# Kernel optimization log

Hardware: AMD Instinct MI355X
Metric: run time of the kernel (lower is better)

The kernel has to match this reference:

```python
import jax, jax.numpy as jnp
import numpy as np

GRID = 32
NUM_VOXELS = GRID ** 3


def setup_inputs() -> dict:
    key = jax.random.key(0)
    k1, k2 = jax.random.split(key)
    B, D, N = 4, 128, 100000
    features = jax.random.normal(k1, (B, D, N), dtype=jnp.float32)
    xyz = jax.random.uniform(k2, (B, N, 3), dtype=jnp.float32)
    return {"features": features, "xyz": xyz}


def reference(features, xyz):
    # features: [B, D, N], xyz: [B, N, 3]
    B, D, N = features.shape
    G, V = GRID, NUM_VOXELS
    xyz_min = jnp.min(xyz, axis=1, keepdims=True)          # [B, 1, 3]
    xyz_max = jnp.max(xyz, axis=1, keepdims=True)          # [B, 1, 3]
    xyz_range = xyz_max - xyz_min + 1e-8
    norm = jnp.clip((xyz - xyz_min) / xyz_range, 0.0, 1.0 - 1e-6)
    vi = jnp.clip(jnp.floor(norm * G).astype(jnp.int32), 0, G - 1)  # [B, N, 3]
    idx = vi[..., 0] * (G * G) + vi[..., 1] * G + vi[..., 2]        # [B, N]

    def per_batch(feat, ix):
        # feat: [D, N], ix: [N]
        counts = jnp.zeros((V,), jnp.int32).at[ix].add(1)
        # scatter-max, include_self=False semantics: init -inf, then
        # empty voxels fall back to 0 (torch leaves initial zeros untouched)
        fmax = jnp.full((V, feat.shape[0]), -jnp.inf, feat.dtype).at[ix].max(feat.T)
        fmax = jnp.where(counts[:, None] == 0, jnp.zeros((), feat.dtype), fmax)
        return counts, fmax.T  # [V], [D, V]

    counts, voxel_features = jax.vmap(per_batch)(features, idx)
    voxel_features_3d = voxel_features.reshape(B, D, G, G, G)
    point_counts = counts[:, None, :].astype(jnp.int64)     # [B, 1, V]
    xyz_min_out = jnp.swapaxes(xyz_min, 1, 2)               # [B, 3, 1]
    xyz_max_out = jnp.swapaxes(xyz_max, 1, 2)
    return (voxel_features_3d, idx, point_counts, xyz_min_out, xyz_max_out)
```

## Files before the change

### kernel.cpp

```cpp
#include <hip/hip_runtime.h>
#include <math.h>

#define GG 32
#define NV (GG * GG * GG)
#define BB 4
#define DD 128

__device__ __forceinline__ unsigned int enc_f(float f) {
    unsigned int u = __float_as_uint(f);
    return (u & 0x80000000u) ? ~u : (u | 0x80000000u);
}
__device__ __forceinline__ float dec_f(unsigned int u) {
    return __uint_as_float((u & 0x80000000u) ? (u ^ 0x80000000u) : ~u);
}
#define ENC_NEG_INF 0x007FFFFFu
#define ENC_POS_INF 0xFF800000u

__global__ void k_init_small(unsigned int* __restrict__ mm) {
    int i = threadIdx.x;
    if (i < BB * 6) mm[i] = ((i % 6) < 3) ? ENC_POS_INF : ENC_NEG_INF;
}

__global__ void k_minmax(const float* __restrict__ xyz,
                         unsigned int* __restrict__ mm,
                         int* __restrict__ cnt, int N) {
    int b = blockIdx.y;
    int tid = threadIdx.x;
    int gid = blockIdx.x * blockDim.x + tid;
    int stride = gridDim.x * blockDim.x;

    int gtid = (blockIdx.y * gridDim.x + blockIdx.x) * blockDim.x + tid;
    int gtot = gridDim.x * gridDim.y * blockDim.x;
    for (int j = gtid; j < BB * NV; j += gtot) cnt[j] = 0;

    float mn[3] = {INFINITY, INFINITY, INFINITY};
    float mx[3] = {-INFINITY, -INFINITY, -INFINITY};
    const float* base = xyz + (size_t)b * N * 3;
    const float4* p4 = (const float4*)base;
    int Ng = N >> 2;
    for (int g = gid; g < Ng; g += stride) {
        float4 a = p4[3 * g];
        float4 c = p4[3 * g + 1];
        float4 e = p4[3 * g + 2];
        mn[0] = fminf(mn[0], fminf(fminf(a.x, a.w), fminf(c.z, e.y)));
        mx[0] = fmaxf(mx[0], fmaxf(fmaxf(a.x, a.w), fmaxf(c.z, e.y)));
        mn[1] = fminf(mn[1], fminf(fminf(a.y, c.x), fminf(c.w, e.z)));
        mx[1] = fmaxf(mx[1], fmaxf(fmaxf(a.y, c.x), fmaxf(c.w, e.z)));
        mn[2] = fminf(mn[2], fminf(fminf(a.z, c.y), fminf(e.x, e.w)));
        mx[2] = fmaxf(mx[2], fmaxf(fmaxf(a.z, c.y), fmaxf(e.x, e.w)));
    }
    for (int n = (Ng << 2) + gid; n < N; n += stride) {
        const float* p = base + (size_t)n * 3;
        #pragma unroll
        for (int k = 0; k < 3; k++) {
            float v = p[k];
            mn[k] = fminf(mn[k], v);
            mx[k] = fmaxf(mx[k], v);
        }
    }
    for (int o = 32; o > 0; o >>= 1) {
        #pragma unroll
        for (int k = 0; k < 3; k++) {
            mn[k] = fminf(mn[k], __shfl_xor(mn[k], o));
            mx[k] = fmaxf(mx[k], __shfl_xor(mx[k], o));
        }
    }
    __shared__ float smn[4][3], smx[4][3];
    int w = tid >> 6;
    if ((tid & 63) == 0) {
        #pragma unroll
        for (int k = 0; k < 3; k++) { smn[w][k] = mn[k]; smx[w][k] = mx[k]; }
    }
    __syncthreads();
    if (tid == 0) {
        #pragma unroll
        for (int k = 0; k < 3; k++) {
            float a = fminf(fminf(smn[0][k], smn[1][k]), fminf(smn[2][k], smn[3][k]));
            float c = fmaxf(fmaxf(smx[0][k], smx[1][k]), fmaxf(smx[2][k], smx[3][k]));
            atomicMin(&mm[b * 6 + k], enc_f(a));
            atomicMax(&mm[b * 6 + 3 + k], enc_f(c));
        }
    }
}

__device__ __forceinline__ int quant_idx(float x, float y, float z,
                                         const float* mnv, const float* mxv) {
    const float CLIP_HI = 1.0f - 1e-6f;
    float p[3] = {x, y, z};
    int vi[3];
    #pragma unroll
    for (int k = 0; k < 3; k++) {
        float rng = (mxv[k] - mnv[k]) + 1e-8f;
        float t = (p[k] - mnv[k]) / rng;
        t = fminf(fmaxf(t, 0.0f), CLIP_HI);
        int q = (int)floorf(t * 32.0f);
        q = min(max(q, 0), GG - 1);
        vi[k] = q;
    }
    return vi[0] * (GG * GG) + vi[1] * GG + vi[2];
}

__global__ void k_idx(const float* __restrict__ xyz,
                      const unsigned int* __restrict__ mm,
                      float* __restrict__ out_idx,
                      int* __restrict__ idx_i,
                      int* __restrict__ cnt, int N) {
    int g = blockIdx.x * blockDim.x + threadIdx.x;
    int b = blockIdx.y;
    float mnv[3], mxv[3];
    #pragma unroll
    for (int k = 0; k < 3; k++) {
        mnv[k] = dec_f(mm[b * 6 + k]);
        mxv[k] = dec_f(mm[b * 6 + 3 + k]);
    }
    int Ng = N >> 2;
    const float4* p4 = (const float4*)(xyz + (size_t)b * N * 3);
    if (g < Ng) {
        float4 a = p4[3 * g];
        float4 c = p4[3 * g + 1];
        float4 e = p4[3 * g + 2];
        int i0 = quant_idx(a.x, a.y, a.z, mnv, mxv);
        int i1 = quant_idx(a.w, c.x, c.y, mnv, mxv);
        int i2 = quant_idx(c.z, c.w, e.x, mnv, mxv);
        int i3 = quant_idx(e.y, e.z, e.w, mnv, mxv);
        size_t o = (size_t)b * N + 4 * (size_t)g;
        *(float4*)(out_idx + o) = make_float4((float)i0, (float)i1,
                                              (float)i2, (float)i3);
        if (idx_i) *(int4*)(idx_i + o) = make_int4(i0, i1, i2, i3);
        atomicAdd(&cnt[b * NV + i0], 1);
        atomicAdd(&cnt[b * NV + i1], 1);
        atomicAdd(&cnt[b * NV + i2], 1);
        atomicAdd(&cnt[b * NV + i3], 1);
    }
    if (g == 0) {
        for (int n = Ng << 2; n < N; n++) {
            const float* p = xyz + ((size_t)b * N + n) * 3;
            int id = quant_idx(p[0], p[1], p[2], mnv, mxv);
            out_idx[(size_t)b * N + n] = (float)id;
            if (idx_i) idx_i[(size_t)b * N + n] = id;
            atomicAdd(&cnt[b * NV + id], 1);
        }
    }
}

__global__ __launch_bounds__(1024) void k_fuse(const float* __restrict__ feat,
                                               const int* __restrict__ idx_i,
                                               float* __restrict__ out, int N,
                                               long off_cnt, long off_mm,
                                               const unsigned int* __restrict__ mm) {
    int d = blockIdx.x;
    int b = blockIdx.y;
    int t = threadIdx.x;
    const int T = 1024;

    if (d == DD) {
        int*   cp = (int*)out + off_cnt + (long)b * NV;
        float4* cf = (float4*)(out + off_cnt + (long)b * NV);
        const int4* ci = (const int4*)cp;
        #pragma unroll
        for (int r = 0; r < NV / 4 / T; r++) {
            int v = r * T + t;
            int4 x = ci[v];
            cf[v] = make_float4((float)x.x, (float)x.y, (float)x.z, (float)x.w);
        }
        if (t < 3) {
            out[off_mm + b * 3 + t]      = dec_f(mm[b * 6 + t]);
            out[off_mm + 12 + b * 3 + t] = dec_f(mm[b * 6 + 3 + t]);
        }
        return;
    }

    __shared__ unsigned int s[NV];
    uint4* s4 = (uint4*)s;
    uint4 sent = make_uint4(ENC_NEG_INF, ENC_NEG_INF, ENC_NEG_INF, ENC_NEG_INF);
    #pragma unroll
    for (int v = 0; v < NV / 4 / T; v++) s4[v * T + t] = sent;
    __syncthreads();

    const float* fp = feat + ((size_t)b * DD + d) * N;
    const int*   ip = idx_i + (size_t)b * N;

    if ((N & 3) == 0) {
        const float4* f4 = (const float4*)fp;
        const int4*   i4 = (const int4*)ip;
        int n4 = N >> 2;
        int nfull = (n4 / (4 * T)) * (4 * T);
        int i = t;
        for (; i < nfull; i += 4 * T) {
            float4 f0 = f4[i];
            float4 f1 = f4[i + T];
            float4 f2 = f4[i + 2 * T];
            float4 f3 = f4[i + 3 * T];
            int4 x0 = i4[i];
            int4 x1 = i4[i + T];
            int4 x2 = i4[i + 2 * T];
            int4 x3 = i4[i + 3 * T];
            atomicMax(&s[x0.x], enc_f(f0.x));
            atomicMax(&s[x0.y], enc_f(f0.y));
            atomicMax(&s[x0.z], enc_f(f0.z));
            atomicMax(&s[x0.w], enc_f(f0.w));
            atomicMax(&s[x1.x], enc_f(f1.x));
            atomicMax(&s[x1.y], enc_f(f1.y));
            atomicMax(&s[x1.z], enc_f(f1.z));
            atomicMax(&s[x1.w], enc_f(f1.w));
            atomicMax(&s[x2.x], enc_f(f2.x));
            atomicMax(&s[x2.y], enc_f(f2.y));
            atomicMax(&s[x2.z], enc_f(f2.z));
            atomicMax(&s[x2.w], enc_f(f2.w));
            atomicMax(&s[x3.x], enc_f(f3.x));
            atomicMax(&s[x3.y], enc_f(f3.y));
            atomicMax(&s[x3.z], enc_f(f3.z));
            atomicMax(&s[x3.w], enc_f(f3.w));
        }
        for (; i < n4; i += T) {
            float4 f = f4[i];
            int4   x = i4[i];
            atomicMax(&s[x.x], enc_f(f.x));
            atomicMax(&s[x.y], enc_f(f.y));
            atomicMax(&s[x.z], enc_f(f.z));
            atomicMax(&s[x.w], enc_f(f.w));
        }
    } else {
        for (int i = t; i < N; i += T) atomicMax(&s[ip[i]], enc_f(fp[i]));
    }
    __syncthreads();

    float4* op = (float4*)(out + ((size_t)b * DD + d) * NV);
    #pragma unroll
    for (int r = 0; r < NV / 4 / T; r++) {
        int v = r * T + t;
        unsigned int u0 = s[4 * v + 0];
        unsigned int u1 = s[4 * v + 1];
        unsigned int u2 = s[4 * v + 2];
        unsigned int u3 = s[4 * v + 3];
        float4 o;
        o.x = (u0 == ENC_NEG_INF) ? 0.0f : dec_f(u0);
        o.y = (u1 == ENC_NEG_INF) ? 0.0f : dec_f(u1);
        o.z = (u2 == ENC_NEG_INF) ? 0.0f : dec_f(u2);
        o.w = (u3 == ENC_NEG_INF) ? 0.0f : dec_f(u3);
        op[v] = o;
    }
}

__global__ void k_fin_tail(float* __restrict__ out,
                           const unsigned int* __restrict__ mm,
                           long off_cnt, long off_mm) {
    int i = blockIdx.x * blockDim.x + threadIdx.x;
    if (i < BB * NV) {
        int c = ((const int*)out)[off_cnt + i];
        out[off_cnt + i] = (float)c;
    }
    if (i < BB * 3) {
        int b = i / 3, k = i % 3;
        out[off_mm + i]      = dec_f(mm[b * 6 + k]);
        out[off_mm + 12 + i] = dec_f(mm[b * 6 + 3 + k]);
    }
}


__global__ void k_init_legacy(unsigned int* __restrict__ out_u, long nvox,
                              unsigned int* __restrict__ mm,
                              unsigned int* __restrict__ cnt, long ncnt) {
    long i = blockIdx.x * (long)blockDim.x + threadIdx.x;
    long stride = gridDim.x * (long)blockDim.x;
    for (long j = i; j < nvox; j += stride) out_u[j] = ENC_NEG_INF;
    for (long j = i; j < ncnt; j += stride) cnt[j] = 0u;
    if (i < BB * 6) mm[i] = ((i % 6) < 3) ? ENC_POS_INF : ENC_NEG_INF;
}

__global__ void k_scatter_legacy(const float* __restrict__ feat,
                                 const float* __restrict__ out_idx,
                                 unsigned int* __restrict__ vox, int N) {
    int n = blockIdx.x * blockDim.x + threadIdx.x;
    int b = blockIdx.y;
    if (n >= N) return;
    int idx = (int)out_idx[(size_t)b * N + n];
    const float* fp = feat + (size_t)b * DD * N + n;
    unsigned int* vp = vox + (size_t)b * DD * NV + idx;
    #pragma unroll 4
    for (int d = 0; d < DD; d++) {
        atomicMax(vp + (size_t)d * NV, enc_f(fp[(size_t)d * N]));
    }
}

__global__ void k_fin_vox_legacy(unsigned int* __restrict__ out_u,
                                 const int* __restrict__ cnt) {
    size_t i = blockIdx.x * (size_t)blockDim.x + threadIdx.x;
    int b = (int)(i >> 22);
    int v = (int)(i & (NV - 1));
    unsigned int u = out_u[i];
    float f = (cnt[b * NV + v] == 0) ? 0.0f : dec_f(u);
    ((float*)out_u)[i] = f;
}

extern "C" void kernel_launch(void* const* d_in, const int* in_sizes, int n_in,
                              void* d_out, int out_size, void* d_ws, size_t ws_size,
                              hipStream_t stream) {
    const float* features = (const float*)d_in[0];
    const float* xyz      = (const float*)d_in[1];
    int N = in_sizes[1] / (BB * 3);

    float* out = (float*)d_out;
    unsigned int* ws_u = (unsigned int*)d_ws;

    const long nvox    = (long)BB * DD * NV;
    const long off_idx = nvox;
    const long off_cnt = off_idx + (long)BB * N;
    const long ncnt    = (long)BB * NV;
    const long off_mm  = off_cnt + ncnt;

    float* out_idx = out + off_idx;
    int*   cnt     = (int*)(out + off_cnt);

    int Ng = N >> 2;
    int nb4 = (Ng + 255) / 256; if (nb4 < 1) nb4 = 1;

    bool fused = ws_size >= (size_t)((long)BB * N + 24) * 4;

    if (fused) {
        int* idx_i = (int*)ws_u;
        unsigned int* mm = (unsigned int*)(idx_i + (long)BB * N);

        k_init_small<<<1, 64, 0, stream>>>(mm);
        k_minmax<<<dim3(64, BB), 256, 0, stream>>>(xyz, mm, cnt, N);
        k_idx<<<dim3(nb4, BB), 256, 0, stream>>>(xyz, mm, out_idx, idx_i, cnt, N);
        k_fuse<<<dim3(DD + 1, BB), 1024, 0, stream>>>(features, idx_i, out, N,
                                                      off_cnt, off_mm, mm);
    } else {
        unsigned int* mm = ws_u;
        k_init_legacy<<<2048, 256, 0, stream>>>((unsigned int*)out, nvox, mm,
                                                (unsigned int*)cnt, ncnt);
        k_minmax<<<dim3(64, BB), 256, 0, stream>>>(xyz, mm, cnt, N);
        k_idx<<<dim3(nb4, BB), 256, 0, stream>>>(xyz, mm, out_idx,
                                                 (int*)NULL, cnt, N);
        k_scatter_legacy<<<dim3((N + 255) / 256, BB), 256, 0, stream>>>(
            features, out_idx, (unsigned int*)out, N);
        k_fin_vox_legacy<<<(unsigned)(nvox / 256), 256, 0, stream>>>(
            (unsigned int*)out, cnt);
        k_fin_tail<<<(int)((ncnt + 255) / 256), 256, 0, stream>>>(out, mm, off_cnt, off_mm);
    }
}
```

Measured before the change: 342.9 us.

## Replace global atomic minmax with per-block partials, add nontemporal IO and conditional atomics

Min/max reduction now writes per-block partials that later kernels reduce themselves, which removes the init kernel and the global atomics. The fuse kernel skips an LDS atomicMax when the current value is already larger, and uses nontemporal loads for features and nontemporal stores for outputs. The 4x-unrolled scatter loop is collapsed into a simple strided loop, and the count/minmax block moves to block 0. The risks are redundant partial reductions in every block and less memory-level parallelism from dropping the unroll.

```diff
diff --git a/kernel.cpp b/kernel.cpp
--- a/kernel.cpp
+++ b/kernel.cpp
@@ -16,13 +16,42 @@
 #define ENC_NEG_INF 0x007FFFFFu
 #define ENC_POS_INF 0xFF800000u
 
-__global__ void k_init_small(unsigned int* __restrict__ mm) {
-    int i = threadIdx.x;
-    if (i < BB * 6) mm[i] = ((i % 6) < 3) ? ENC_POS_INF : ENC_NEG_INF;
+typedef float        __attribute__((ext_vector_type(4))) f32x4;
+typedef int          __attribute__((ext_vector_type(4))) i32x4;
+typedef unsigned int __attribute__((ext_vector_type(4))) u32x4;
+
+__device__ __forceinline__ float4 nt_loadf4(const float* p) {
+    f32x4 v = __builtin_nontemporal_load((const f32x4*)p);
+    return make_float4(v.x, v.y, v.z, v.w);
+}
+__device__ __forceinline__ void nt_storef4(float* p, float4 v) {
+    f32x4 t = {v.x, v.y, v.z, v.w};
+    __builtin_nontemporal_store(t, (f32x4*)p);
+}
+
+__device__ __forceinline__ void reduce_partials(const float* __restrict__ part,
+                                                int b, float* sm, int tid) {
+    if (tid < 64) {
+        float v[6];
+        #pragma unroll
+        for (int k = 0; k < 6; k++) v[k] = part[(b * 64 + tid) * 6 + k];
+        for (int o = 32; o > 0; o >>= 1) {
+            #pragma unroll
+            for (int k = 0; k < 3; k++) {
+                v[k]     = fminf(v[k],     __shfl_xor(v[k],     o));
+                v[k + 3] = fmaxf(v[k + 3], __shfl_xor(v[k + 3], o));
+            }
+        }
+        if (tid == 0) {
+            #pragma unroll
+            for (int k = 0; k < 6; k++) sm[k] = v[k];
+        }
+    }
+    __syncthreads();
 }
 
 __global__ void k_minmax(const float* __restrict__ xyz,
-                         unsigned int* __restrict__ mm,
+                         float* __restrict__ part,
                          int* __restrict__ cnt, int N) {
     int b = blockIdx.y;
     int tid = threadIdx.x;
@@ -73,12 +102,11 @@
     }
     __syncthreads();
     if (tid == 0) {
-        #pragma unroll
-        for (int k = 0; k < 3; k++) {
-            float a = fminf(fminf(smn[0][k], smn[1][k]), fminf(smn[2][k], smn[3][k]));
-            float c = fmaxf(fmaxf(smx[0][k], smx[1][k]), fmaxf(smx[2][k], smx[3][k]));
-            atomicMin(&mm[b * 6 + k], enc_f(a));
-            atomicMax(&mm[b * 6 + 3 + k], enc_f(c));
+        float* pb = part + ((size_t)b * 64 + blockIdx.x) * 6;
+        #pragma unroll
+        for (int k = 0; k < 3; k++) {
+            pb[k]     = fminf(fminf(smn[0][k], smn[1][k]), fminf(smn[2][k], smn[3][k]));
+            pb[3 + k] = fmaxf(fmaxf(smx[0][k], smx[1][k]), fmaxf(smx[2][k], smx[3][k]));
         }
     }
 }
@@ -101,18 +129,17 @@
 }
 
 __global__ void k_idx(const float* __restrict__ xyz,
-                      const unsigned int* __restrict__ mm,
+                      const float* __restrict__ part,
                       float* __restrict__ out_idx,
                       int* __restrict__ idx_i,
                       int* __restrict__ cnt, int N) {
     int g = blockIdx.x * blockDim.x + threadIdx.x;
     int b = blockIdx.y;
-    float mnv[3], mxv[3];
-    #pragma unroll
-    for (int k = 0; k < 3; k++) {
-        mnv[k] = dec_f(mm[b * 6 + k]);
-        mxv[k] = dec_f(mm[b * 6 + 3 + k]);
-    }
+    __shared__ float sm[6];
+    reduce_partials(part, b, sm, threadIdx.x);
+    float mnv[3] = {sm[0], sm[1], sm[2]};
+    float mxv[3] = {sm[3], sm[4], sm[5]};
+
     int Ng = N >> 2;
     const float4* p4 = (const float4*)(xyz + (size_t)b * N * 3);
     if (g < Ng) {
@@ -124,8 +151,8 @@
         int i2 = quant_idx(c.z, c.w, e.x, mnv, mxv);
         int i3 = quant_idx(e.y, e.z, e.w, mnv, mxv);
         size_t o = (size_t)b * N + 4 * (size_t)g;
-        *(float4*)(out_idx + o) = make_float4((float)i0, (float)i1,
-                                              (float)i2, (float)i3);
+        nt_storef4(out_idx + o, make_float4((float)i0, (float)i1,
+                                            (float)i2, (float)i3));
         if (idx_i) *(int4*)(idx_i + o) = make_int4(i0, i1, i2, i3);
         atomicAdd(&cnt[b * NV + i0], 1);
         atomicAdd(&cnt[b * NV + i1], 1);
@@ -147,14 +174,15 @@
                                                const int* __restrict__ idx_i,
                                                float* __restrict__ out, int N,
                                                long off_cnt, long off_mm,
-                                               const unsigned int* __restrict__ mm) {
-    int d = blockIdx.x;
+                                               const float* __restrict__ part) {
     int b = blockIdx.y;
     int t = threadIdx.x;
     const int T = 1024;
-
-    if (d == DD) {
-        int*   cp = (int*)out + off_cnt + (long)b * NV;
+    __shared__ unsigned int s[NV];
+    __shared__ float sm[6];
+
+    if (blockIdx.x == 0) {
+        int*    cp = (int*)out + off_cnt + (long)b * NV;
         float4* cf = (float4*)(out + off_cnt + (long)b * NV);
         const int4* ci = (const int4*)cp;
         #pragma unroll
@@ -163,14 +191,15 @@
             int4 x = ci[v];
             cf[v] = make_float4((float)x.x, (float)x.y, (float)x.z, (float)x.w);
         }
+        reduce_partials(part, b, sm, t);
         if (t < 3) {
-            out[off_mm + b * 3 + t]      = dec_f(mm[b * 6 + t]);
-            out[off_mm + 12 + b * 3 + t] = dec_f(mm[b * 6 + 3 + t]);
+            out[off_mm + b * 3 + t]      = sm[t];
+            out[off_mm + 12 + b * 3 + t] = sm[3 + t];
         }
         return;
     }
-
-    __shared__ unsigned int s[NV];
+    int d = blockIdx.x - 1;
+
     uint4* s4 = (uint4*)s;
     uint4 sent = make_uint4(ENC_NEG_INF, ENC_NEG_INF, ENC_NEG_INF, ENC_NEG_INF);
     #pragma unroll
@@ -181,51 +210,29 @@
     const int*   ip = idx_i + (size_t)b * N;
 
     if ((N & 3) == 0) {
-        const float4* f4 = (const float4*)fp;
-        const int4*   i4 = (const int4*)ip;
+        const int4* i4 = (const int4*)ip;
         int n4 = N >> 2;
-        int nfull = (n4 / (4 * T)) * (4 * T);
-        int i = t;
-        for (; i < nfull; i += 4 * T) {
-            float4 f0 = f4[i];
-            float4 f1 = f4[i + T];
-            float4 f2 = f4[i + 2 * T];
-            float4 f3 = f4[i + 3 * T];
-            int4 x0 = i4[i];
-            int4 x1 = i4[i + T];
-            int4 x2 = i4[i + 2 * T];
-            int4 x3 = i4[i + 3 * T];
-            atomicMax(&s[x0.x], enc_f(f0.x));
-            atomicMax(&s[x0.y], enc_f(f0.y));
-            atomicMax(&s[x0.z], enc_f(f0.z));
-            atomicMax(&s[x0.w], enc_f(f0.w));
-            atomicMax(&s[x1.x], enc_f(f1.x));
-            atomicMax(&s[x1.y], enc_f(f1.y));
-            atomicMax(&s[x1.z], enc_f(f1.z));
-            atomicMax(&s[x1.w], enc_f(f1.w));
-            atomicMax(&s[x2.x], enc_f(f2.x));
-            atomicMax(&s[x2.y], enc_f(f2.y));
-            atomicMax(&s[x2.z], enc_f(f2.z));
-            atomicMax(&s[x2.w], enc_f(f2.w));
-            atomicMax(&s[x3.x], enc_f(f3.x));
-            atomicMax(&s[x3.y], enc_f(f3.y));
-            atomicMax(&s[x3.z], enc_f(f3.z));
-            atomicMax(&s[x3.w], enc_f(f3.w));
-        }
-        for (; i < n4; i += T) {
-            float4 f = f4[i];
+        for (int i = t; i < n4; i += T) {
+            float4 f = nt_loadf4(fp + 4 * (size_t)i);
             int4   x = i4[i];
-            atomicMax(&s[x.x], enc_f(f.x));
-            atomicMax(&s[x.y], enc_f(f.y));
-            atomicMax(&s[x.z], enc_f(f.z));
-            atomicMax(&s[x.w], enc_f(f.w));
+            unsigned int e0 = enc_f(f.x);
+            unsigned int e1 = enc_f(f.y);
+            unsigned int e2 = enc_f(f.z);
+            unsigned int e3 = enc_f(f.w);
+            if (e0 > s[x.x]) atomicMax(&s[x.x], e0);
+            if (e1 > s[x.y]) atomicMax(&s[x.y], e1);
+            if (e2 > s[x.z]) atomicMax(&s[x.z], e2);
+            if (e3 > s[x.w]) atomicMax(&s[x.w], e3);
         }
     } else {
-        for (int i = t; i < N; i += T) atomicMax(&s[ip[i]], enc_f(fp[i]));
+        for (int i = t; i < N; i += T) {
+            unsigned int e = enc_f(fp[i]);
+            if (e > s[ip[i]]) atomicMax(&s[ip[i]], e);
+        }
     }
     __syncthreads();
 
-    float4* op = (float4*)(out + ((size_t)b * DD + d) * NV);
+    float* op = out + ((size_t)b * DD + d) * NV;
     #pragma unroll
     for (int r = 0; r < NV / 4 / T; r++) {
         int v = r * T + t;
@@ -238,25 +245,73 @@
         o.y = (u1 == ENC_NEG_INF) ? 0.0f : dec_f(u1);
         o.z = (u2 == ENC_NEG_INF) ? 0.0f : dec_f(u2);
         o.w = (u3 == ENC_NEG_INF) ? 0.0f : dec_f(u3);
-        op[v] = o;
-    }
-}
-
-__global__ void k_fin_tail(float* __restrict__ out,
-                           const unsigned int* __restrict__ mm,
-                           long off_cnt, long off_mm) {
-    int i = blockIdx.x * blockDim.x + threadIdx.x;
-    if (i < BB * NV) {
-        int c = ((const int*)out)[off_cnt + i];
-        out[off_cnt + i] = (float)c;
-    }
-    if (i < BB * 3) {
-        int b = i / 3, k = i % 3;
-        out[off_mm + i]      = dec_f(mm[b * 6 + k]);
-        out[off_mm + 12 + i] = dec_f(mm[b * 6 + 3 + k]);
-    }
-}
-
+        nt_storef4(op + 4 * (size_t)v, o);
+    }
+}
+
+
+__global__ void k_minmax_legacy(const float* __restrict__ xyz,
+                                unsigned int* __restrict__ mm,
+                                int* __restrict__ cnt, int N) {
+    int b = blockIdx.y;
+    int tid = threadIdx.x;
+    int gid = blockIdx.x * blockDim.x + tid;
+    int stride = gridDim.x * blockDim.x;
+    float mn[3] = {INFINITY, INFINITY, INFINITY};
+    float mx[3] = {-INFINITY, -INFINITY, -INFINITY};
+    const float* base = xyz + (size_t)b * N * 3;
+    for (int n = gid; n < N; n += stride) {
+        const float* p = base + (size_t)n * 3;
+        #pragma unroll
+        for (int k = 0; k < 3; k++) {
+            float v = p[k];
+            mn[k] = fminf(mn[k], v);
+            mx[k] = fmaxf(mx[k], v);
+        }
+    }
+    for (int o = 32; o > 0; o >>= 1) {
+        #pragma unroll
+        for (int k = 0; k < 3; k++) {
+            mn[k] = fminf(mn[k], __shfl_xor(mn[k], o));
+            mx[k] = fmaxf(mx[k], __shfl_xor(mx[k], o));
+        }
+    }
+    __shared__ float smn[4][3], smx[4][3];
+    int w = tid >> 6;
+    if ((tid & 63) == 0) {
+        #pragma unroll
+        for (int k = 0; k < 3; k++) { smn[w][k] = mn[k]; smx[w][k] = mx[k]; }
+    }
+    __syncthreads();
+    if (tid == 0) {
+        #pragma unroll
+        for (int k = 0; k < 3; k++) {
+            float a = fminf(fminf(smn[0][k], smn[1][k]), fminf(smn[2][k], smn[3][k]));
+            float c = fmaxf(fmaxf(smx[0][k], smx[1][k]), fmaxf(smx[2][k], smx[3][k]));
+            atomicMin(&mm[b * 6 + k], enc_f(a));
+            atomicMax(&mm[b * 6 + 3 + k], enc_f(c));
+        }
+    }
+}
+
+__global__ void k_idx_legacy(const float* __restrict__ xyz,
+                             const unsigned int* __restrict__ mm,
+                             float* __restrict__ out_idx,
+                             int* __restrict__ cnt, int N) {
+    int n = blockIdx.x * blockDim.x + threadIdx.x;
+    int b = blockIdx.y;
+    if (n >= N) return;
+    float mnv[3], mxv[3];
+    #pragma unroll
+    for (int k = 0; k < 3; k++) {
+        mnv[k] = dec_f(mm[b * 6 + k]);
+        mxv[k] = dec_f(mm[b * 6 + 3 + k]);
+    }
+    const float* p = xyz + ((size_t)b * N + n) * 3;
+    int idx = quant_idx(p[0], p[1], p[2], mnv, mxv);
+    out_idx[(size_t)b * N + n] = (float)idx;
+    atomicAdd(&cnt[b * NV + idx], 1);
+}
 
 __global__ void k_init_legacy(unsigned int* __restrict__ out_u, long nvox,
                               unsigned int* __restrict__ mm,
@@ -293,6 +348,21 @@
     ((float*)out_u)[i] = f;
 }
 
+__global__ void k_fin_tail_legacy(float* __restrict__ out,
+                                  const unsigned int* __restrict__ mm,
+                                  long off_cnt, long off_mm) {
+    int i = blockIdx.x * blockDim.x + threadIdx.x;
+    if (i < BB * NV) {
+        int c = ((const int*)out)[off_cnt + i];
+        out[off_cnt + i] = (float)c;
+    }
+    if (i < BB * 3) {
+        int b = i / 3, k = i % 3;
+        out[off_mm + i]      = dec_f(mm[b * 6 + k]);
+        out[off_mm + 12 + i] = dec_f(mm[b * 6 + 3 + k]);
+    }
+}
+
 extern "C" void kernel_launch(void* const* d_in, const int* in_sizes, int n_in,
                               void* d_out, int out_size, void* d_ws, size_t ws_size,
                               hipStream_t stream) {
@@ -315,28 +385,28 @@
     int Ng = N >> 2;
     int nb4 = (Ng + 255) / 256; if (nb4 < 1) nb4 = 1;
 
-    bool fused = ws_size >= (size_t)((long)BB * N + 24) * 4;
+    bool fused = ws_size >= (size_t)((long)BB * N + (long)BB * 64 * 6) * 4;
 
     if (fused) {
-        int* idx_i = (int*)ws_u;
-        unsigned int* mm = (unsigned int*)(idx_i + (long)BB * N);
-
-        k_init_small<<<1, 64, 0, stream>>>(mm);
-        k_minmax<<<dim3(64, BB), 256, 0, stream>>>(xyz, mm, cnt, N);
-        k_idx<<<dim3(nb4, BB), 256, 0, stream>>>(xyz, mm, out_idx, idx_i, cnt, N);
+        int*   idx_i = (int*)ws_u;
+        float* part  = (float*)(idx_i + (long)BB * N);
+
+        k_minmax<<<dim3(64, BB), 256, 0, stream>>>(xyz, part, cnt, N);
+        k_idx<<<dim3(nb4, BB), 256, 0, stream>>>(xyz, part, out_idx, idx_i, cnt, N);
         k_fuse<<<dim3(DD + 1, BB), 1024, 0, stream>>>(features, idx_i, out, N,
-                                                      off_cnt, off_mm, mm);
+                                                      off_cnt, off_mm, part);
     } else {
         unsigned int* mm = ws_u;
         k_init_legacy<<<2048, 256, 0, stream>>>((unsigned int*)out, nvox, mm,
                                                 (unsigned int*)cnt, ncnt);
-        k_minmax<<<dim3(64, BB), 256, 0, stream>>>(xyz, mm, cnt, N);
-        k_idx<<<dim3(nb4, BB), 256, 0, stream>>>(xyz, mm, out_idx,
-                                                 (int*)NULL, cnt, N);
+        k_minmax_legacy<<<dim3(64, BB), 256, 0, stream>>>(xyz, mm, cnt, N);
+        k_idx_legacy<<<dim3((N + 255) / 256, BB), 256, 0, stream>>>(
+            xyz, mm, out_idx, cnt, N);
         k_scatter_legacy<<<dim3((N + 255) / 256, BB), 256, 0, stream>>>(
             features, out_idx, (unsigned int*)out, N);
         k_fin_vox_legacy<<<(unsigned)(nvox / 256), 256, 0, stream>>>(
             (unsigned int*)out, cnt);
-        k_fin_tail<<<(int)((ncnt + 255) / 256), 256, 0, stream>>>(out, mm, off_cnt, off_mm);
-    }
-}
+        k_fin_tail_legacy<<<(int)((ncnt + 255) / 256), 256, 0, stream>>>(
+            out, mm, off_cnt, off_mm);
+    }
+}
```

New measurement: 320.6 us. 1.07x faster.
